# Kernel tuning notes

Hardware: AMD Instinct MI355X
Metric: run time of the kernel (lower is better)

## Reference

```python
import jax, jax.numpy as jnp
import numpy as np

D_MODEL = 1024
N_HEADS = 16
D_K = D_MODEL // N_HEADS


def setup_inputs() -> dict:
    key = jax.random.key(0)
    ks = jax.random.split(key, 12)
    B, S, D = 4, 2048, D_MODEL
    scale = 1.0 / np.sqrt(D)
    inp = {
        'query': jax.random.normal(ks[0], (B, S, D), jnp.float32),
        'key': jax.random.normal(ks[1], (B, S, D), jnp.float32),
        'value': jax.random.normal(ks[2], (B, S, D), jnp.float32),
        'Wq': jax.random.normal(ks[3], (D, D), jnp.float32) * scale,
        'bq': jax.random.normal(ks[4], (D,), jnp.float32) * 0.02,
        'Wk': jax.random.normal(ks[5], (D, D), jnp.float32) * scale,
        'bk': jax.random.normal(ks[6], (D,), jnp.float32) * 0.02,
        'Wv': jax.random.normal(ks[7], (D, D), jnp.float32) * scale,
        'bv': jax.random.normal(ks[8], (D,), jnp.float32) * 0.02,
        'Wo': jax.random.normal(ks[9], (D, D), jnp.float32) * scale,
        'bo': jax.random.normal(ks[10], (D,), jnp.float32) * 0.02,
    }
    return inp


def reference(query, key, value, Wq, bq, Wk, bk, Wv, bv, Wo, bo):
    B, S, D = query.shape
    # torch nn.Linear: y = x @ W^T + b
    def proj(x, W, b):
        y = jnp.einsum('bsd,ed->bse', x, W) + b
        # [B,S,D] -> [B,H,S,d_k]
        return y.reshape(B, S, N_HEADS, D_K).transpose(0, 2, 1, 3)

    q = proj(query, Wq, bq)
    k = proj(key, Wk, bk)
    v = proj(value, Wv, bv)

    scores = jnp.einsum('bhqd,bhkd->bhqk', q, k) / jnp.sqrt(jnp.float32(D_K))
    attn = jax.nn.softmax(scores, axis=-1)  # dropout = identity (eval mode)
    out = jnp.einsum('bhqk,bhkd->bhqd', attn, v)
    out = out.transpose(0, 2, 1, 3).reshape(B, S, D)
    return jnp.einsum('bsd,ed->bse', out, Wo) + bo
```

## Files before the change

### kernel.cpp

```cpp
#include <hip/hip_runtime.h>
#include <hip/hip_bf16.h>
#include <cstdint>
#include <cstddef>


#define BATCH   4
#define SEQ     2048
#define D_MODEL 1024
#define NHEADS  16
#define DK      64

typedef __attribute__((ext_vector_type(8)))  __bf16 bf16x8_t;
typedef __attribute__((ext_vector_type(4)))  float  f32x4;
typedef __attribute__((ext_vector_type(16))) float  f32x16;

__device__ inline unsigned int pack2(float lo, float hi) {
  __hip_bfloat162 h = __float22bfloat162_rn(make_float2(lo, hi));
  union { __hip_bfloat162 h; unsigned int u; } c; c.h = h; return c.u;
}
__device__ inline unsigned short f2bf(float f) { return (unsigned short)pack2(f, f); }

#if __has_builtin(__builtin_amdgcn_exp2f)
__device__ inline float fexp2(float x) { return __builtin_amdgcn_exp2f(x); }
#else
__device__ inline float fexp2(float x) { return __expf(x * 0.6931471805599453f); }
#endif

__device__ inline unsigned int exch32(unsigned int x) {
  return (unsigned int)__shfl_xor((int)x, 32);
}

__device__ inline void cvt8(const float* __restrict__ s, unsigned short* __restrict__ d) {
  const float4 a = *(const float4*)s;
  const float4 b = *(const float4*)(s + 4);
  uint4 r;
  r.x = pack2(a.x, a.y); r.y = pack2(a.z, a.w);
  r.z = pack2(b.x, b.y); r.w = pack2(b.z, b.w);
  *(uint4*)d = r;
}

typedef __attribute__((address_space(3))) unsigned int lds_u32_t;
typedef const __attribute__((address_space(1))) unsigned int glb_u32_t;
__device__ inline void gld16(const unsigned short* g, unsigned short* l) {
  __builtin_amdgcn_global_load_lds((glb_u32_t*)(uintptr_t)g,
                                   (lds_u32_t*)(unsigned int)(uintptr_t)l, 16, 0, 0);
}

__global__ __launch_bounds__(256) void cvt7_kernel(
    const float* __restrict__ a, const float* __restrict__ b, const float* __restrict__ c,
    const float* __restrict__ w0, const float* __restrict__ w1,
    const float* __restrict__ w2, const float* __restrict__ w3,
    unsigned short* __restrict__ oa, unsigned short* __restrict__ ob, unsigned short* __restrict__ oc,
    unsigned short* __restrict__ ow0, unsigned short* __restrict__ ow1,
    unsigned short* __restrict__ ow2, unsigned short* __restrict__ ow3)
{
  const int bx = blockIdx.x;
  const float* s;
  unsigned short* d;
  size_t local;
  if (bx < 12288) {
    const int t = bx >> 12;
    local = (size_t)(bx & 4095);
    s = (t == 0) ? a : (t == 1) ? b : c;
    d = (t == 0) ? oa : (t == 1) ? ob : oc;
  } else {
    const int t = (bx - 12288) >> 9;
    local = (size_t)((bx - 12288) & 511);
    s = (t == 0) ? w0 : (t == 1) ? w1 : (t == 2) ? w2 : w3;
    d = (t == 0) ? ow0 : (t == 1) ? ow1 : (t == 2) ? ow2 : ow3;
  }
  const size_t i = (local * 256 + threadIdx.x) * 8;
  cvt8(s + i, d + i);
}

template <bool SWAP>
__device__ inline void gemm_core(const unsigned short* __restrict__ A,
                                 const unsigned short* __restrict__ W,
                                 unsigned short* a_lds, unsigned short* b_lds,
                                 int m0, int n0, f32x4 (&acc)[4][4])
{
  const int tid  = threadIdx.x;
  const int lane = tid & 63;
  const int wv   = tid >> 6;
  const int l15  = lane & 15;
  const int quad = lane >> 4;
  const int wm = (wv & 1) * 64;
  const int wn = (wv >> 1) * 64;

  const int srow = tid >> 2;
  const int sch  = (tid & 3) ^ (srow & 3);
  const unsigned short* Ap0 = A + (size_t)(m0 + srow) * D_MODEL + sch * 8;
  const unsigned short* Ap1 = Ap0 + (size_t)64 * D_MODEL;
  const unsigned short* Wp0 = W + (size_t)(n0 + srow) * D_MODEL + sch * 8;
  const unsigned short* Wp1 = Wp0 + (size_t)64 * D_MODEL;
  unsigned short* al0 = a_lds + wv * 512;
  unsigned short* al1 = a_lds + 2048 + wv * 512;
  unsigned short* bl0 = b_lds + wv * 512;
  unsigned short* bl1 = b_lds + 2048 + wv * 512;

  const int pq = (quad ^ (l15 & 3)) * 8;

  for (int k0 = 0; k0 < D_MODEL; k0 += 32) {
    __syncthreads();
    gld16(Ap0 + k0, al0);
    gld16(Ap1 + k0, al1);
    gld16(Wp0 + k0, bl0);
    gld16(Wp1 + k0, bl1);
    __syncthreads();

    bf16x8_t af[4], bfr[4];
#pragma unroll
    for (int i = 0; i < 4; ++i)
      af[i] = *(const bf16x8_t*)&a_lds[(wm + i * 16 + l15) * 32 + pq];
#pragma unroll
    for (int j = 0; j < 4; ++j)
      bfr[j] = *(const bf16x8_t*)&b_lds[(wn + j * 16 + l15) * 32 + pq];

#pragma unroll
    for (int i = 0; i < 4; ++i)
#pragma unroll
      for (int j = 0; j < 4; ++j) {
        if constexpr (SWAP)
          acc[i][j] = __builtin_amdgcn_mfma_f32_16x16x32_bf16(bfr[j], af[i], acc[i][j], 0, 0, 0);
        else
          acc[i][j] = __builtin_amdgcn_mfma_f32_16x16x32_bf16(af[i], bfr[j], acc[i][j], 0, 0, 0);
      }
  }
}

__global__ __launch_bounds__(256) void qkv_kernel(
    const unsigned short* __restrict__ qb, const unsigned short* __restrict__ kb,
    const unsigned short* __restrict__ vb,
    const unsigned short* __restrict__ wq, const unsigned short* __restrict__ wk,
    const unsigned short* __restrict__ wvp,
    const float* __restrict__ bq, const float* __restrict__ bk, const float* __restrict__ bv,
    unsigned short* __restrict__ Qws, unsigned short* __restrict__ Kws,
    unsigned short* __restrict__ Vws)
{
  __shared__ unsigned short a_lds[128 * 32];
  __shared__ unsigned short b_lds[128 * 32];

  const int z = blockIdx.z;
  const unsigned short* A = (z == 0) ? qb : (z == 1) ? kb : vb;
  const unsigned short* W = (z == 0) ? wq : (z == 1) ? wk : wvp;
  const float* bias       = (z == 0) ? bq : (z == 1) ? bk : bv;
  unsigned short* C       = (z == 0) ? Qws : (z == 1) ? Kws : Vws;
  const int m0 = blockIdx.x * 128;
  const int n0 = blockIdx.y * 128;

  f32x4 acc[4][4];
#pragma unroll
  for (int i = 0; i < 4; ++i)
#pragma unroll
    for (int j = 0; j < 4; ++j)
      acc[i][j] = (f32x4){0.f, 0.f, 0.f, 0.f};

  const int tid  = threadIdx.x;
  const int lane = tid & 63;
  const int wv   = tid >> 6;
  const int l15  = lane & 15;
  const int quad = lane >> 4;
  const int wm = (wv & 1) * 64;
  const int wn = (wv >> 1) * 64;

  if (z == 2) {
    gemm_core<false>(A, W, a_lds, b_lds, m0, n0, acc);
    for (int j = 0; j < 4; ++j) {
      const int n = n0 + wn + j * 16 + l15;
      const int hh = n >> 6, dd = n & 63;
      const float bvl = bias[n];
      for (int i = 0; i < 4; ++i) {
        const int mbase = m0 + wm + i * 16 + quad * 4;
        const int bb = mbase >> 11, ss = mbase & 2047;
        uint2 w2 = make_uint2(pack2(acc[i][j][0] + bvl, acc[i][j][1] + bvl),
                              pack2(acc[i][j][2] + bvl, acc[i][j][3] + bvl));
        *(uint2*)(C + (((size_t)bb * NHEADS + hh) * DK + dd) * SEQ + ss) = w2;
      }
    }
  } else {
    gemm_core<true>(A, W, a_lds, b_lds, m0, n0, acc);
    const float oscale = (z == 0) ? 0.18033688011112042f : 1.0f;
    for (int j = 0; j < 4; ++j) {
      const int nb = n0 + wn + j * 16 + quad * 4;
      const int hh = nb >> 6, dd = nb & 63;
      const float4 b4 = *(const float4*)(bias + nb);
      for (int i = 0; i < 4; ++i) {
        const int m = m0 + wm + i * 16 + l15;
        const int bb = m >> 11, ss = m & 2047;
        uint2 w2 = make_uint2(pack2((acc[i][j][0] + b4.x) * oscale, (acc[i][j][1] + b4.y) * oscale),
                              pack2((acc[i][j][2] + b4.z) * oscale, (acc[i][j][3] + b4.w) * oscale));
        *(uint2*)(C + (((size_t)bb * NHEADS + hh) * SEQ + ss) * DK + dd) = w2;
      }
    }
  }
}

__global__ __launch_bounds__(256) void outproj_kernel(
    const unsigned short* __restrict__ A, const unsigned short* __restrict__ W,
    const float* __restrict__ bias, float* __restrict__ C)
{
  __shared__ unsigned short a_lds[128 * 32];
  __shared__ unsigned short b_lds[128 * 32];
  const int m0 = blockIdx.x * 128;
  const int n0 = blockIdx.y * 128;

  f32x4 acc[4][4];
#pragma unroll
  for (int i = 0; i < 4; ++i)
#pragma unroll
    for (int j = 0; j < 4; ++j)
      acc[i][j] = (f32x4){0.f, 0.f, 0.f, 0.f};

  gemm_core<true>(A, W, a_lds, b_lds, m0, n0, acc);

  const int tid  = threadIdx.x;
  const int lane = tid & 63;
  const int wv   = tid >> 6;
  const int l15  = lane & 15;
  const int quad = lane >> 4;
  const int wm = (wv & 1) * 64;
  const int wn = (wv >> 1) * 64;
  for (int j = 0; j < 4; ++j) {
    const int nb = n0 + wn + j * 16 + quad * 4;
    const float4 b4 = *(const float4*)(bias + nb);
    for (int i = 0; i < 4; ++i) {
      const int m = m0 + wm + i * 16 + l15;
      float4 o4 = make_float4(acc[i][j][0] + b4.x, acc[i][j][1] + b4.y,
                              acc[i][j][2] + b4.z, acc[i][j][3] + b4.w);
      *(float4*)(C + (size_t)m * D_MODEL + nb) = o4;
    }
  }
}

__global__ __launch_bounds__(512, 4) void attn_kernel(
    const unsigned short* __restrict__ Q,
    const unsigned short* __restrict__ K,
    const unsigned short* __restrict__ Vt,
    unsigned short* __restrict__ Oattn)
{
  __shared__ unsigned short k_sw[2 * 64 * 64];
  __shared__ unsigned short vt_sw[2 * 64 * 64];

  const int tid  = threadIdx.x;
  const int lane = tid & 63;
  const int wv   = tid >> 6;
  const int l31  = lane & 31;
  const int hb   = lane >> 5;
  const int bh   = blockIdx.x;
  const int q0   = blockIdx.y * 256;
  const size_t hoff = (size_t)bh * SEQ * DK;
  const unsigned short* Qh  = Q  + hoff;
  const unsigned short* Kh  = K  + hoff;
  const unsigned short* Vth = Vt + hoff;

  bf16x8_t qf[4];
  {
    const unsigned short* qr = Qh + (size_t)(q0 + wv * 32 + l31) * DK;
#pragma unroll
    for (int kk = 0; kk < 4; ++kk)
      qf[kk] = *(const bf16x8_t*)(qr + kk * 16 + hb * 8);
  }

  f32x16 oAcc[2];
#pragma unroll
  for (int dh = 0; dh < 2; ++dh)
#pragma unroll
    for (int i = 0; i < 16; ++i) oAcc[dh][i] = 0.f;
  float mval = -1e30f, lval = 0.f;

  const int sr  = lane >> 3;
  const int pc  = lane & 7;
  const int row = wv * 8 + sr;
  const int sem = pc ^ sr ^ wv;
  const unsigned short* KsA = Kh  + (size_t)row * DK  + sem * 8;
  const unsigned short* VsA = Vth + (size_t)row * SEQ + sem * 8;
  unsigned short* kd = k_sw  + wv * 512;
  unsigned short* vd = vt_sw + wv * 512;

#define STAGE(buf, key0) do {                                        \
    gld16(KsA + (size_t)(key0) * DK, kd + (buf) * 4096);             \
    gld16(VsA + (key0),              vd + (buf) * 4096);             \
  } while (0)

  STAGE(0, 0);
  __syncthreads();

  const int swr0 = (l31 & 7) ^ (l31 >> 3);
  const int swr1 = (l31 & 7) ^ ((l31 >> 3) ^ 4);

  int cur = 0;
  for (int kb = 0; kb < SEQ / 64; ++kb) {
    if (kb + 1 < SEQ / 64) STAGE(cur ^ 1, (kb + 1) * 64);

    const unsigned short* kcur = k_sw  + cur * 4096;
    const unsigned short* vcur = vt_sw + cur * 4096;

    f32x16 s0, s1;
#pragma unroll
    for (int i = 0; i < 16; ++i) { s0[i] = 0.f; s1[i] = 0.f; }
    __builtin_amdgcn_s_setprio(1);
    {
      const unsigned short* krow = kcur + l31 * 64;
#pragma unroll
      for (int kk = 0; kk < 4; ++kk) {
        bf16x8_t kf = *(const bf16x8_t*)&krow[((2 * kk + hb) ^ swr0) << 3];
        s0 = __builtin_amdgcn_mfma_f32_32x32x16_bf16(kf, qf[kk], s0, 0, 0, 0);
      }
    }
    {
      const unsigned short* krow = kcur + (32 + l31) * 64;
#pragma unroll
      for (int kk = 0; kk < 4; ++kk) {
        bf16x8_t kf = *(const bf16x8_t*)&krow[((2 * kk + hb) ^ swr1) << 3];
        s1 = __builtin_amdgcn_mfma_f32_32x32x16_bf16(kf, qf[kk], s1, 0, 0, 0);
      }
    }
    __builtin_amdgcn_s_setprio(0);

    float mx = s0[0];
#pragma unroll
    for (int i = 1; i < 16; ++i) mx = fmaxf(mx, s0[i]);
#pragma unroll
    for (int i = 0; i < 16; ++i) mx = fmaxf(mx, s1[i]);
    mx = fmaxf(mx, __shfl_xor(mx, 32));
    if (__any(mx > mval + 8.0f)) {
      const float mnew  = fmaxf(mval, mx);
      const float alpha = fexp2(mval - mnew);
      mval = mnew;
      lval *= alpha;
#pragma unroll
      for (int dh = 0; dh < 2; ++dh)
#pragma unroll
        for (int i = 0; i < 16; ++i) oAcc[dh][i] *= alpha;
    }
    float rs = 0.f;
    unsigned int w0[8], w1[8];
#pragma unroll
    for (int m = 0; m < 8; ++m) {
      const float p0 = fexp2(s0[2 * m] - mval);
      const float p1 = fexp2(s0[2 * m + 1] - mval);
      rs += p0 + p1;
      w0[m] = pack2(p0, p1);
    }
#pragma unroll
    for (int m = 0; m < 8; ++m) {
      const float p0 = fexp2(s1[2 * m] - mval);
      const float p1 = fexp2(s1[2 * m + 1] - mval);
      rs += p0 + p1;
      w1[m] = pack2(p0, p1);
    }
    rs += __shfl_xor(rs, 32);
    lval += rs;

    union Cv { unsigned int w[4]; bf16x8_t v; };
    bf16x8_t pf[4];
    {
      const unsigned int e0 = exch32(w0[0]), e1 = exch32(w0[1]);
      const unsigned int e2 = exch32(w0[2]), e3 = exch32(w0[3]);
      Cv c;
      c.w[0] = hb ? e2 : w0[0]; c.w[1] = hb ? e3 : w0[1];
      c.w[2] = hb ? w0[2] : e0; c.w[3] = hb ? w0[3] : e1;
      pf[0] = c.v;
    }
    {
      const unsigned int e0 = exch32(w0[4]), e1 = exch32(w0[5]);
      const unsigned int e2 = exch32(w0[6]), e3 = exch32(w0[7]);
      Cv c;
      c.w[0] = hb ? e2 : w0[4]; c.w[1] = hb ? e3 : w0[5];
      c.w[2] = hb ? w0[6] : e0; c.w[3] = hb ? w0[7] : e1;
      pf[1] = c.v;
    }
    {
      const unsigned int e0 = exch32(w1[0]), e1 = exch32(w1[1]);
      const unsigned int e2 = exch32(w1[2]), e3 = exch32(w1[3]);
      Cv c;
      c.w[0] = hb ? e2 : w1[0]; c.w[1] = hb ? e3 : w1[1];
      c.w[2] = hb ? w1[2] : e0; c.w[3] = hb ? w1[3] : e1;
      pf[2] = c.v;
    }
    {
      const unsigned int e0 = exch32(w1[4]), e1 = exch32(w1[5]);
      const unsigned int e2 = exch32(w1[6]), e3 = exch32(w1[7]);
      Cv c;
      c.w[0] = hb ? e2 : w1[4]; c.w[1] = hb ? e3 : w1[5];
      c.w[2] = hb ? w1[6] : e0; c.w[3] = hb ? w1[7] : e1;
      pf[3] = c.v;
    }

    __builtin_amdgcn_s_setprio(1);
    {
      const unsigned short* vrow = vcur + l31 * 64;
#pragma unroll
      for (int t = 0; t < 4; ++t) {
        bf16x8_t vf = *(const bf16x8_t*)&vrow[((2 * t + hb) ^ swr0) << 3];
        oAcc[0] = __builtin_amdgcn_mfma_f32_32x32x16_bf16(vf, pf[t], oAcc[0], 0, 0, 0);
      }
    }
    {
      const unsigned short* vrow = vcur + (32 + l31) * 64;
#pragma unroll
      for (int t = 0; t < 4; ++t) {
        bf16x8_t vf = *(const bf16x8_t*)&vrow[((2 * t + hb) ^ swr1) << 3];
        oAcc[1] = __builtin_amdgcn_mfma_f32_32x32x16_bf16(vf, pf[t], oAcc[1], 0, 0, 0);
      }
    }
    __builtin_amdgcn_s_setprio(0);

    __syncthreads();
    cur ^= 1;
  }
#undef STAGE

  const int bb = bh >> 4, hh = bh & 15;
  const float inv = 1.0f / lval;
  unsigned short* orow = Oattn + (size_t)(bb * SEQ + q0 + wv * 32 + l31) * D_MODEL
                       + hh * DK + hb * 4;
#pragma unroll
  for (int dh = 0; dh < 2; ++dh)
#pragma unroll
    for (int a = 0; a < 4; ++a) {
      const float v0 = oAcc[dh][4 * a]     * inv;
      const float v1 = oAcc[dh][4 * a + 1] * inv;
      const float v2 = oAcc[dh][4 * a + 2] * inv;
      const float v3 = oAcc[dh][4 * a + 3] * inv;
      *(uint2*)(orow + dh * 32 + a * 8) = make_uint2(pack2(v0, v1), pack2(v2, v3));
    }
}

extern "C" void kernel_launch(void* const* d_in, const int* in_sizes, int n_in,
                              void* d_out, int out_size, void* d_ws, size_t ws_size,
                              hipStream_t stream) {
  const float* query = (const float*)d_in[0];
  const float* key   = (const float*)d_in[1];
  const float* value = (const float*)d_in[2];
  const float* Wq    = (const float*)d_in[3];
  const float* bq    = (const float*)d_in[4];
  const float* Wk    = (const float*)d_in[5];
  const float* bk    = (const float*)d_in[6];
  const float* Wv    = (const float*)d_in[7];
  const float* bv    = (const float*)d_in[8];
  const float* Wo    = (const float*)d_in[9];
  const float* bo    = (const float*)d_in[10];

  const size_t E  = (size_t)BATCH * SEQ * D_MODEL;
  const size_t WE = (size_t)D_MODEL * D_MODEL;
  unsigned short* ws  = (unsigned short*)d_ws;
  unsigned short* Qws = ws;
  unsigned short* Kws = ws + E;
  unsigned short* Vws = ws + 2 * E;
  unsigned short* qb  = ws + 3 * E;
  unsigned short* kb  = ws + 4 * E;
  unsigned short* vb  = ws + 5 * E;
  unsigned short* wqb = ws + 6 * E;
  unsigned short* wkb = wqb + WE;
  unsigned short* wvb = wqb + 2 * WE;
  unsigned short* wob = wqb + 3 * WE;
  unsigned short* Aws = qb;

  cvt7_kernel<<<dim3(12288 + 2048), 256, 0, stream>>>(
      query, key, value, Wq, Wk, Wv, Wo, qb, kb, vb, wqb, wkb, wvb, wob);

  qkv_kernel<<<dim3(BATCH * SEQ / 128, D_MODEL / 128, 3), 256, 0, stream>>>(
      qb, kb, vb, wqb, wkb, wvb, bq, bk, bv, Qws, Kws, Vws);
  attn_kernel<<<dim3(BATCH * NHEADS, SEQ / 256), 512, 0, stream>>>(Qws, Kws, Vws, Aws);
  outproj_kernel<<<dim3(BATCH * SEQ / 128, D_MODEL / 128), 256, 0, stream>>>(
      Aws, wob, bo, (float*)d_out);
}
```

Measured before the change: 351.3 us.

## Double-buffer LDS tiles in GEMM core to overlap global loads with MFMA

The shared GEMM core used by the QKV and output projection kernels now keeps two LDS buffers. The next K-tile is prefetched into the alternate buffer while MFMAs run on the current one, which replaces two barriers per iteration with one. The aim is to hide global-to-LDS load latency behind compute. It doubles LDS per block, which may lower occupancy. It also relies on the gld16 async loads having completed by the time the single barrier is reached.

```diff
diff --git a/kernel.cpp b/kernel.cpp
--- a/kernel.cpp
+++ b/kernel.cpp
@@ -93,28 +93,34 @@
   const unsigned short* Ap1 = Ap0 + (size_t)64 * D_MODEL;
   const unsigned short* Wp0 = W + (size_t)(n0 + srow) * D_MODEL + sch * 8;
   const unsigned short* Wp1 = Wp0 + (size_t)64 * D_MODEL;
-  unsigned short* al0 = a_lds + wv * 512;
-  unsigned short* al1 = a_lds + 2048 + wv * 512;
-  unsigned short* bl0 = b_lds + wv * 512;
-  unsigned short* bl1 = b_lds + 2048 + wv * 512;
+  const int dst0 = wv * 512;
+  const int dst1 = 2048 + wv * 512;
+
+#define GSTAGE(buf, k0) do {                                  \
+    gld16(Ap0 + (k0), a_lds + (buf) * 4096 + dst0);           \
+    gld16(Ap1 + (k0), a_lds + (buf) * 4096 + dst1);           \
+    gld16(Wp0 + (k0), b_lds + (buf) * 4096 + dst0);           \
+    gld16(Wp1 + (k0), b_lds + (buf) * 4096 + dst1);           \
+  } while (0)
 
   const int pq = (quad ^ (l15 & 3)) * 8;
 
+  GSTAGE(0, 0);
+  __syncthreads();
+
+  int cur = 0;
   for (int k0 = 0; k0 < D_MODEL; k0 += 32) {
-    __syncthreads();
-    gld16(Ap0 + k0, al0);
-    gld16(Ap1 + k0, al1);
-    gld16(Wp0 + k0, bl0);
-    gld16(Wp1 + k0, bl1);
-    __syncthreads();
-
+    if (k0 + 32 < D_MODEL) GSTAGE(cur ^ 1, k0 + 32);
+
+    const unsigned short* al = a_lds + cur * 4096;
+    const unsigned short* bl = b_lds + cur * 4096;
     bf16x8_t af[4], bfr[4];
 #pragma unroll
     for (int i = 0; i < 4; ++i)
-      af[i] = *(const bf16x8_t*)&a_lds[(wm + i * 16 + l15) * 32 + pq];
+      af[i] = *(const bf16x8_t*)&al[(wm + i * 16 + l15) * 32 + pq];
 #pragma unroll
     for (int j = 0; j < 4; ++j)
-      bfr[j] = *(const bf16x8_t*)&b_lds[(wn + j * 16 + l15) * 32 + pq];
+      bfr[j] = *(const bf16x8_t*)&bl[(wn + j * 16 + l15) * 32 + pq];
 
 #pragma unroll
     for (int i = 0; i < 4; ++i)
@@ -125,7 +131,11 @@
         else
           acc[i][j] = __builtin_amdgcn_mfma_f32_16x16x32_bf16(af[i], bfr[j], acc[i][j], 0, 0, 0);
       }
-  }
+
+    __syncthreads();
+    cur ^= 1;
+  }
+#undef GSTAGE
 }
 
 __global__ __launch_bounds__(256) void qkv_kernel(
@@ -137,8 +147,8 @@
     unsigned short* __restrict__ Qws, unsigned short* __restrict__ Kws,
     unsigned short* __restrict__ Vws)
 {
-  __shared__ unsigned short a_lds[128 * 32];
-  __shared__ unsigned short b_lds[128 * 32];
+  __shared__ unsigned short a_lds[2 * 128 * 32];
+  __shared__ unsigned short b_lds[2 * 128 * 32];
 
   const int z = blockIdx.z;
   const unsigned short* A = (z == 0) ? qb : (z == 1) ? kb : vb;
@@ -199,8 +209,8 @@
     const unsigned short* __restrict__ A, const unsigned short* __restrict__ W,
     const float* __restrict__ bias, float* __restrict__ C)
 {
-  __shared__ unsigned short a_lds[128 * 32];
-  __shared__ unsigned short b_lds[128 * 32];
+  __shared__ unsigned short a_lds[2 * 128 * 32];
+  __shared__ unsigned short b_lds[2 * 128 * 32];
   const int m0 = blockIdx.x * 128;
   const int n0 = blockIdx.y * 128;
 
```

Result: slower. 361.8 us (+3.0%).

## Process two 32-query groups per wave in attention kernel

Applied to the files above, without the earlier changes.

Each wave now handles 64 query rows as two independent 32-row groups instead of one, with the block shrunk from 512 to 256 threads over the same 256-query tile. Each K and V fragment read from LDS then feeds two MFMAs, which halves LDS read traffic per FLOP and gives the scheduler independent work to interleave. The staging loads per thread double to keep the same tile. The cost is much higher register pressure, with a second set of score and output accumulators and softmax state, and launch bounds lowered to 2 blocks per CU, which may reduce occupancy or cause spills.

```diff
diff --git a/kernel.cpp b/kernel.cpp
--- a/kernel.cpp
+++ b/kernel.cpp
@@ -232,7 +232,63 @@
   }
 }
 
-__global__ __launch_bounds__(512, 4) void attn_kernel(
+__device__ inline void softmax_group(const f32x16& s0, const f32x16& s1,
+                                     float& mval, float& lval, f32x16 (&o)[2],
+                                     bf16x8_t (&pf)[4], const int hb)
+{
+  float mx = s0[0];
+#pragma unroll
+  for (int i = 1; i < 16; ++i) mx = fmaxf(mx, s0[i]);
+#pragma unroll
+  for (int i = 0; i < 16; ++i) mx = fmaxf(mx, s1[i]);
+  mx = fmaxf(mx, __shfl_xor(mx, 32));
+  if (__any(mx > mval + 8.0f)) {
+    const float mnew  = fmaxf(mval, mx);
+    const float alpha = fexp2(mval - mnew);
+    mval = mnew;
+    lval *= alpha;
+#pragma unroll
+    for (int dh = 0; dh < 2; ++dh)
+#pragma unroll
+      for (int i = 0; i < 16; ++i) o[dh][i] *= alpha;
+  }
+  float rs = 0.f;
+  unsigned int w0[8], w1[8];
+#pragma unroll
+  for (int m = 0; m < 8; ++m) {
+    const float p0 = fexp2(s0[2 * m] - mval);
+    const float p1 = fexp2(s0[2 * m + 1] - mval);
+    rs += p0 + p1;
+    w0[m] = pack2(p0, p1);
+  }
+#pragma unroll
+  for (int m = 0; m < 8; ++m) {
+    const float p0 = fexp2(s1[2 * m] - mval);
+    const float p1 = fexp2(s1[2 * m + 1] - mval);
+    rs += p0 + p1;
+    w1[m] = pack2(p0, p1);
+  }
+  rs += __shfl_xor(rs, 32);
+  lval += rs;
+
+  union Cv { unsigned int w[4]; bf16x8_t v; };
+#pragma unroll
+  for (int f = 0; f < 4; ++f) {
+    const unsigned int* w = (f < 2) ? (w0 + 4 * f) : (w1 + 4 * (f - 2));
+    const unsigned int t0 = hb ? w[0] : w[2];
+    const unsigned int t1 = hb ? w[1] : w[3];
+    const unsigned int x0 = exch32(t0);
+    const unsigned int x1 = exch32(t1);
+    Cv c;
+    c.w[0] = hb ? x0 : w[0];
+    c.w[1] = hb ? x1 : w[1];
+    c.w[2] = hb ? w[2] : x0;
+    c.w[3] = hb ? w[3] : x1;
+    pf[f] = c.v;
+  }
+}
+
+__global__ __launch_bounds__(256, 2) void attn_kernel(
     const unsigned short* __restrict__ Q,
     const unsigned short* __restrict__ K,
     const unsigned short* __restrict__ Vt,
@@ -253,33 +309,43 @@
   const unsigned short* Kh  = K  + hoff;
   const unsigned short* Vth = Vt + hoff;
 
-  bf16x8_t qf[4];
+  bf16x8_t qfA[4], qfB[4];
   {
-    const unsigned short* qr = Qh + (size_t)(q0 + wv * 32 + l31) * DK;
-#pragma unroll
-    for (int kk = 0; kk < 4; ++kk)
-      qf[kk] = *(const bf16x8_t*)(qr + kk * 16 + hb * 8);
-  }
-
-  f32x16 oAcc[2];
+    const unsigned short* qrA = Qh + (size_t)(q0 + wv * 64 + l31) * DK;
+    const unsigned short* qrB = qrA + (size_t)32 * DK;
+#pragma unroll
+    for (int kk = 0; kk < 4; ++kk) {
+      qfA[kk] = *(const bf16x8_t*)(qrA + kk * 16 + hb * 8);
+      qfB[kk] = *(const bf16x8_t*)(qrB + kk * 16 + hb * 8);
+    }
+  }
+
+  f32x16 oA[2], oB[2];
 #pragma unroll
   for (int dh = 0; dh < 2; ++dh)
 #pragma unroll
-    for (int i = 0; i < 16; ++i) oAcc[dh][i] = 0.f;
-  float mval = -1e30f, lval = 0.f;
+    for (int i = 0; i < 16; ++i) { oA[dh][i] = 0.f; oB[dh][i] = 0.f; }
+  float mA = -1e30f, lA = 0.f;
+  float mB = -1e30f, lB = 0.f;
 
   const int sr  = lane >> 3;
   const int pc  = lane & 7;
-  const int row = wv * 8 + sr;
-  const int sem = pc ^ sr ^ wv;
-  const unsigned short* KsA = Kh  + (size_t)row * DK  + sem * 8;
-  const unsigned short* VsA = Vth + (size_t)row * SEQ + sem * 8;
-  unsigned short* kd = k_sw  + wv * 512;
-  unsigned short* vd = vt_sw + wv * 512;
+  const int r0  = wv * 16 + sr;
+  const int r1  = r0 + 8;
+  const int sem0 = pc ^ sr ^ (2 * wv);
+  const int sem1 = pc ^ sr ^ (2 * wv + 1);
+  const unsigned short* KsA = Kh  + (size_t)r0 * DK  + sem0 * 8;
+  const unsigned short* KsB = Kh  + (size_t)r1 * DK  + sem1 * 8;
+  const unsigned short* VsA = Vth + (size_t)r0 * SEQ + sem0 * 8;
+  const unsigned short* VsB = Vth + (size_t)r1 * SEQ + sem1 * 8;
+  unsigned short* kd = k_sw  + wv * 1024;
+  unsigned short* vd = vt_sw + wv * 1024;
 
 #define STAGE(buf, key0) do {                                        \
     gld16(KsA + (size_t)(key0) * DK, kd + (buf) * 4096);             \
+    gld16(KsB + (size_t)(key0) * DK, kd + (buf) * 4096 + 512);       \
     gld16(VsA + (key0),              vd + (buf) * 4096);             \
+    gld16(VsB + (key0),              vd + (buf) * 4096 + 512);       \
   } while (0)
 
   STAGE(0, 0);
@@ -295,16 +361,17 @@
     const unsigned short* kcur = k_sw  + cur * 4096;
     const unsigned short* vcur = vt_sw + cur * 4096;
 
-    f32x16 s0, s1;
-#pragma unroll
-    for (int i = 0; i < 16; ++i) { s0[i] = 0.f; s1[i] = 0.f; }
+    f32x16 sA0, sA1, sB0, sB1;
+#pragma unroll
+    for (int i = 0; i < 16; ++i) { sA0[i] = 0.f; sA1[i] = 0.f; sB0[i] = 0.f; sB1[i] = 0.f; }
     __builtin_amdgcn_s_setprio(1);
     {
       const unsigned short* krow = kcur + l31 * 64;
 #pragma unroll
       for (int kk = 0; kk < 4; ++kk) {
         bf16x8_t kf = *(const bf16x8_t*)&krow[((2 * kk + hb) ^ swr0) << 3];
-        s0 = __builtin_amdgcn_mfma_f32_32x32x16_bf16(kf, qf[kk], s0, 0, 0, 0);
+        sA0 = __builtin_amdgcn_mfma_f32_32x32x16_bf16(kf, qfA[kk], sA0, 0, 0, 0);
+        sB0 = __builtin_amdgcn_mfma_f32_32x32x16_bf16(kf, qfB[kk], sB0, 0, 0, 0);
       }
     }
     {
@@ -312,80 +379,15 @@
 #pragma unroll
       for (int kk = 0; kk < 4; ++kk) {
         bf16x8_t kf = *(const bf16x8_t*)&krow[((2 * kk + hb) ^ swr1) << 3];
-        s1 = __builtin_amdgcn_mfma_f32_32x32x16_bf16(kf, qf[kk], s1, 0, 0, 0);
+        sA1 = __builtin_amdgcn_mfma_f32_32x32x16_bf16(kf, qfA[kk], sA1, 0, 0, 0);
+        sB1 = __builtin_amdgcn_mfma_f32_32x32x16_bf16(kf, qfB[kk], sB1, 0, 0, 0);
       }
     }
     __builtin_amdgcn_s_setprio(0);
 
-    float mx = s0[0];
-#pragma unroll
-    for (int i = 1; i < 16; ++i) mx = fmaxf(mx, s0[i]);
-#pragma unroll
-    for (int i = 0; i < 16; ++i) mx = fmaxf(mx, s1[i]);
-    mx = fmaxf(mx, __shfl_xor(mx, 32));
-    if (__any(mx > mval + 8.0f)) {
-      const float mnew  = fmaxf(mval, mx);
-      const float alpha = fexp2(mval - mnew);
-      mval = mnew;
-      lval *= alpha;
-#pragma unroll
-      for (int dh = 0; dh < 2; ++dh)
-#pragma unroll
-        for (int i = 0; i < 16; ++i) oAcc[dh][i] *= alpha;
-    }
-    float rs = 0.f;
-    unsigned int w0[8], w1[8];
-#pragma unroll
-    for (int m = 0; m < 8; ++m) {
-      const float p0 = fexp2(s0[2 * m] - mval);
-      const float p1 = fexp2(s0[2 * m + 1] - mval);
-      rs += p0 + p1;
-      w0[m] = pack2(p0, p1);
-    }
-#pragma unroll
-    for (int m = 0; m < 8; ++m) {
-      const float p0 = fexp2(s1[2 * m] - mval);
-      const float p1 = fexp2(s1[2 * m + 1] - mval);
-      rs += p0 + p1;
-      w1[m] = pack2(p0, p1);
-    }
-    rs += __shfl_xor(rs, 32);
-    lval += rs;
-
-    union Cv { unsigned int w[4]; bf16x8_t v; };
-    bf16x8_t pf[4];
-    {
-      const unsigned int e0 = exch32(w0[0]), e1 = exch32(w0[1]);
-      const unsigned int e2 = exch32(w0[2]), e3 = exch32(w0[3]);
-      Cv c;
-      c.w[0] = hb ? e2 : w0[0]; c.w[1] = hb ? e3 : w0[1];
-      c.w[2] = hb ? w0[2] : e0; c.w[3] = hb ? w0[3] : e1;
-      pf[0] = c.v;
-    }
-    {
-      const unsigned int e0 = exch32(w0[4]), e1 = exch32(w0[5]);
-      const unsigned int e2 = exch32(w0[6]), e3 = exch32(w0[7]);
-      Cv c;
-      c.w[0] = hb ? e2 : w0[4]; c.w[1] = hb ? e3 : w0[5];
-      c.w[2] = hb ? w0[6] : e0; c.w[3] = hb ? w0[7] : e1;
-      pf[1] = c.v;
-    }
-    {
-      const unsigned int e0 = exch32(w1[0]), e1 = exch32(w1[1]);
-      const unsigned int e2 = exch32(w1[2]), e3 = exch32(w1[3]);
-      Cv c;
-      c.w[0] = hb ? e2 : w1[0]; c.w[1] = hb ? e3 : w1[1];
-      c.w[2] = hb ? w1[2] : e0; c.w[3] = hb ? w1[3] : e1;
-      pf[2] = c.v;
-    }
-    {
-      const unsigned int e0 = exch32(w1[4]), e1 = exch32(w1[5]);
-      const unsigned int e2 = exch32(w1[6]), e3 = exch32(w1[7]);
-      Cv c;
-      c.w[0] = hb ? e2 : w1[4]; c.w[1] = hb ? e3 : w1[5];
-      c.w[2] = hb ? w1[6] : e0; c.w[3] = hb ? w1[7] : e1;
-      pf[3] = c.v;
-    }
+    bf16x8_t pfA[4], pfB[4];
+    softmax_group(sA0, sA1, mA, lA, oA, pfA, hb);
+    softmax_group(sB0, sB1, mB, lB, oB, pfB, hb);
 
     __builtin_amdgcn_s_setprio(1);
     {
@@ -393,7 +395,8 @@
 #pragma unroll
       for (int t = 0; t < 4; ++t) {
         bf16x8_t vf = *(const bf16x8_t*)&vrow[((2 * t + hb) ^ swr0) << 3];
-        oAcc[0] = __builtin_amdgcn_mfma_f32_32x32x16_bf16(vf, pf[t], oAcc[0], 0, 0, 0);
+        oA[0] = __builtin_amdgcn_mfma_f32_32x32x16_bf16(vf, pfA[t], oA[0], 0, 0, 0);
+        oB[0] = __builtin_amdgcn_mfma_f32_32x32x16_bf16(vf, pfB[t], oB[0], 0, 0, 0);
       }
     }
     {
@@ -401,7 +404,8 @@
 #pragma unroll
       for (int t = 0; t < 4; ++t) {
         bf16x8_t vf = *(const bf16x8_t*)&vrow[((2 * t + hb) ^ swr1) << 3];
-        oAcc[1] = __builtin_amdgcn_mfma_f32_32x32x16_bf16(vf, pf[t], oAcc[1], 0, 0, 0);
+        oA[1] = __builtin_amdgcn_mfma_f32_32x32x16_bf16(vf, pfA[t], oA[1], 0, 0, 0);
+        oB[1] = __builtin_amdgcn_mfma_f32_32x32x16_bf16(vf, pfB[t], oB[1], 0, 0, 0);
       }
     }
     __builtin_amdgcn_s_setprio(0);
@@ -412,19 +416,36 @@
 #undef STAGE
 
   const int bb = bh >> 4, hh = bh & 15;
-  const float inv = 1.0f / lval;
-  unsigned short* orow = Oattn + (size_t)(bb * SEQ + q0 + wv * 32 + l31) * D_MODEL
-                       + hh * DK + hb * 4;
-#pragma unroll
-  for (int dh = 0; dh < 2; ++dh)
-#pragma unroll
-    for (int a = 0; a < 4; ++a) {
-      const float v0 = oAcc[dh][4 * a]     * inv;
-      const float v1 = oAcc[dh][4 * a + 1] * inv;
-      const float v2 = oAcc[dh][4 * a + 2] * inv;
-      const float v3 = oAcc[dh][4 * a + 3] * inv;
-      *(uint2*)(orow + dh * 32 + a * 8) = make_uint2(pack2(v0, v1), pack2(v2, v3));
-    }
+  {
+    const float inv = 1.0f / lA;
+    unsigned short* orow = Oattn + (size_t)(bb * SEQ + q0 + wv * 64 + l31) * D_MODEL
+                         + hh * DK + hb * 4;
+#pragma unroll
+    for (int dh = 0; dh < 2; ++dh)
+#pragma unroll
+      for (int a = 0; a < 4; ++a) {
+        const float v0 = oA[dh][4 * a]     * inv;
+        const float v1 = oA[dh][4 * a + 1] * inv;
+        const float v2 = oA[dh][4 * a + 2] * inv;
+        const float v3 = oA[dh][4 * a + 3] * inv;
+        *(uint2*)(orow + dh * 32 + a * 8) = make_uint2(pack2(v0, v1), pack2(v2, v3));
+      }
+  }
+  {
+    const float inv = 1.0f / lB;
+    unsigned short* orow = Oattn + (size_t)(bb * SEQ + q0 + wv * 64 + 32 + l31) * D_MODEL
+                         + hh * DK + hb * 4;
+#pragma unroll
+    for (int dh = 0; dh < 2; ++dh)
+#pragma unroll
+      for (int a = 0; a < 4; ++a) {
+        const float v0 = oB[dh][4 * a]     * inv;
+        const float v1 = oB[dh][4 * a + 1] * inv;
+        const float v2 = oB[dh][4 * a + 2] * inv;
+        const float v3 = oB[dh][4 * a + 3] * inv;
+        *(uint2*)(orow + dh * 32 + a * 8) = make_uint2(pack2(v0, v1), pack2(v2, v3));
+      }
+  }
 }
 
 extern "C" void kernel_launch(void* const* d_in, const int* in_sizes, int n_in,
@@ -462,7 +483,7 @@
 
   qkv_kernel<<<dim3(BATCH * SEQ / 128, D_MODEL / 128, 3), 256, 0, stream>>>(
       qb, kb, vb, wqb, wkb, wvb, bq, bk, bv, Qws, Kws, Vws);
-  attn_kernel<<<dim3(BATCH * NHEADS, SEQ / 256), 512, 0, stream>>>(Qws, Kws, Vws, Aws);
+  attn_kernel<<<dim3(BATCH * NHEADS, SEQ / 256), 256, 0, stream>>>(Qws, Kws, Vws, Aws);
   outproj_kernel<<<dim3(BATCH * SEQ / 128, D_MODEL / 128), 256, 0, stream>>>(
       Aws, wob, bo, (float*)d_out);
 }
```

After: 365.5 us. 1.04x slower.
